# Kernel tuning notes

Hardware: AMD Instinct MI355X
Metric: run time of the kernel (lower is better)

## Reference

```python
import jax, jax.numpy as jnp
import numpy as np

TEMPERATURE = 0.5  # init kwarg; forward's temperature arg is unused in the original

def _l2norm(x, eps=1e-12):
    # matches F.normalize(dim=-1)
    n = jnp.sqrt(jnp.sum(x * x, axis=-1, keepdims=True))
    return x / jnp.maximum(n, eps)

def setup_inputs() -> dict:
    key = jax.random.key(0)
    k1, k2 = jax.random.split(key)
    h1 = jax.random.normal(k1, (8192, 128), dtype=jnp.float32)
    h2 = jax.random.normal(k2, (8192, 128), dtype=jnp.float32)
    return {"h1": h1, "h2": h2}

def reference(h1, h2):
    t = TEMPERATURE
    h1n = _l2norm(h1)
    h2n = _l2norm(h2)
    h = jnp.concatenate([h1n, h2n], axis=0)              # [2N, d]
    sim = jnp.exp(jnp.matmul(h, h.T) / t)                # [2N, 2N]
    # masked_select of off-diagonal then row-sum == full row-sum minus diagonal
    denom = jnp.sum(sim, axis=-1) - jnp.diagonal(sim)    # [2N]
    pos = jnp.exp(jnp.sum(h1n * h2n, axis=-1) / t)       # [N]
    pos = jnp.concatenate([pos, pos], axis=0)            # [2N]
    loss = -jnp.log(pos / denom)
    return jnp.mean(loss)
```

## Files before the change

kernel.cpp:

```cpp
#include <hip/hip_runtime.h>
#include <hip/hip_bf16.h>

#define N_ROWS 8192
#define DIM    128
#define TWO_N  16384
#define NBLK   64
#define NTRI   (NBLK * (NBLK + 1) / 2)
#define CT     32
#define NT_SQ  8
#define EXP_TWO 7.38905609893065f
#define H_SCALE 1.6986436f

typedef __attribute__((ext_vector_type(8))) short short8;
typedef __attribute__((ext_vector_type(4))) float float4v;

__device__ inline void async_copy16(const void* g, void* l) {
  __builtin_amdgcn_global_load_lds(
      (const __attribute__((address_space(1))) void*)g,
      (__attribute__((address_space(3))) void*)l, 16, 0, 0);
}

__device__ inline float fast_exp2(float x) {
#if __has_builtin(__builtin_amdgcn_exp2f)
  return __builtin_amdgcn_exp2f(x);
#else
  return exp2f(x);
#endif
}

__global__ __launch_bounds__(256) void norm_kernel(
    const float* __restrict__ h1, const float* __restrict__ h2,
    __hip_bfloat16* __restrict__ Hb, float* __restrict__ posdot,
    float* __restrict__ rowsum) {
  if (threadIdx.x < 8) rowsum[blockIdx.x * 8 + threadIdx.x] = 0.0f;

  int lane = threadIdx.x & 63;
  int w    = threadIdx.x >> 6;
  int row  = blockIdx.x * 4 + w;

  const float2* p1 = (const float2*)(h1 + (size_t)row * DIM);
  const float2* p2 = (const float2*)(h2 + (size_t)row * DIM);
  float2 v1 = p1[lane];
  float2 v2 = p2[lane];

  float ss1 = v1.x * v1.x + v1.y * v1.y;
  float ss2 = v2.x * v2.x + v2.y * v2.y;
  #pragma unroll
  for (int m = 32; m; m >>= 1) {
    ss1 += __shfl_xor(ss1, m);
    ss2 += __shfl_xor(ss2, m);
  }
  float inv1 = 1.0f / fmaxf(sqrtf(ss1), 1e-12f);
  float inv2 = 1.0f / fmaxf(sqrtf(ss2), 1e-12f);

  float ax = v1.x * inv1, ay = v1.y * inv1;
  float bx = v2.x * inv2, by = v2.y * inv2;

  float pd = ax * bx + ay * by;
  #pragma unroll
  for (int m = 32; m; m >>= 1) pd += __shfl_xor(pd, m);

  __hip_bfloat162* o1 = (__hip_bfloat162*)(Hb + (size_t)row * DIM);
  __hip_bfloat162* o2 = (__hip_bfloat162*)(Hb + (size_t)(row + N_ROWS) * DIM);
  __hip_bfloat162 t1, t2;
  t1.x = __float2bfloat16(ax * H_SCALE); t1.y = __float2bfloat16(ay * H_SCALE);
  t2.x = __float2bfloat16(bx * H_SCALE); t2.y = __float2bfloat16(by * H_SCALE);
  o1[lane] = t1;
  o2[lane] = t2;

  if (lane == 0) posdot[row] = pd;
}

__global__ __launch_bounds__(256, 2) void ntx_main(
    const __hip_bfloat16* __restrict__ Hb, float* __restrict__ rowsum) {
  __shared__ short smem[2 * 4096];
  __shared__ float colacc[4][256];
  const short* H = (const short*)Hb;

  int tid  = threadIdx.x;
  int lane = tid & 63;
  int w    = tid >> 6;
  int q    = lane >> 4;
  int m    = lane & 15;

  int t = blockIdx.x;
  int I = (int)((129.0f - sqrtf(129.0f * 129.0f - 8.0f * (float)t)) * 0.5f);
  while ((I + 1) * (129 - (I + 1)) / 2 <= t) ++I;
  while (I * (129 - I) / 2 > t) --I;
  int J = I + (t - I * (129 - I) / 2);
  bool diag = (I == J);

  int rowbase = I * 256 + w * 64;
  int colbase = J * 256;

  short8 a[4][4];
  #pragma unroll
  for (int r = 0; r < 4; ++r)
    #pragma unroll
    for (int s = 0; s < 4; ++s)
      a[r][s] = *(const short8*)(H + (size_t)(rowbase + r * 16 + m) * DIM + s * 32 + q * 8);
  #pragma unroll
  for (int r = 0; r < 4; ++r)
    #pragma unroll
    for (int s = 0; s < 4; ++s)
      asm volatile("" : "+v"(a[r][s]));

  float rowacc[4][4];
  #pragma unroll
  for (int r = 0; r < 4; ++r)
    #pragma unroll
    for (int i = 0; i < 4; ++i) rowacc[r][i] = 0.0f;

  int i0 = tid, i1 = tid + 256;
  int c0 = i0 >> 8, s0 = (i0 >> 6) & 3, f0 = i0 & 15, q0 = (i0 >> 4) & 3;
  int c1 = i1 >> 8, s1 = (i1 >> 6) & 3, f1 = i1 & 15, q1 = (i1 >> 4) & 3;
  const short* ga = H + (size_t)(colbase + c0 * 16 + f0) * DIM + s0 * 32 + q0 * 8;
  const short* gb = H + (size_t)(colbase + c1 * 16 + f1) * DIM + s1 * 32 + q1 * 8;

  async_copy16(ga, (void*)&smem[i0 * 8]);
  async_copy16(gb, (void*)&smem[i1 * 8]);
  __syncthreads();

  int buf = 0;
  for (int ct = 0; ct < NT_SQ; ++ct) {
    if (ct + 1 < NT_SQ) {
      ga += CT * DIM;
      gb += CT * DIM;
      int d = (buf ^ 1) * 4096;
      async_copy16(ga, (void*)&smem[d + i0 * 8]);
      async_copy16(gb, (void*)&smem[d + i1 * 8]);
    }

    const short* bsrc = &smem[buf * 4096];
    #pragma unroll
    for (int c = 0; c < 2; ++c) {
      short8 b[4];
      #pragma unroll
      for (int s = 0; s < 4; ++s)
        b[s] = *(const short8*)&bsrc[(c * 256 + s * 64 + lane) * 8];
      float cp = 0.0f;
      #pragma unroll
      for (int r = 0; r < 4; ++r) {
        float4v acc = {0.f, 0.f, 0.f, 0.f};
        #pragma unroll
        for (int s = 0; s < 4; ++s)
          acc = __builtin_amdgcn_mfma_f32_16x16x32_bf16(a[r][s], b[s], acc, 0, 0, 0);
        #pragma unroll
        for (int i = 0; i < 4; ++i) {
          float e = fast_exp2(acc[i]);
          rowacc[r][i] += e;
          cp += e;
        }
      }
      if (!diag) {
        cp += __shfl_xor(cp, 16);
        cp += __shfl_xor(cp, 32);
        if (q == 0) colacc[w][ct * 32 + c * 16 + m] = cp;
      }
    }
    __syncthreads();
    buf ^= 1;
  }

  #pragma unroll
  for (int r = 0; r < 4; ++r)
    #pragma unroll
    for (int i = 0; i < 4; ++i) {
      float v = rowacc[r][i];
      v += __shfl_xor(v, 1);
      v += __shfl_xor(v, 2);
      v += __shfl_xor(v, 4);
      v += __shfl_xor(v, 8);
      rowacc[r][i] = v;
    }
  if (m == 0) {
    #pragma unroll
    for (int r = 0; r < 4; ++r)
      #pragma unroll
      for (int i = 0; i < 4; ++i)
        atomicAdd(&rowsum[rowbase + r * 16 + q * 4 + i], rowacc[r][i]);
  }

  if (!diag) {
    float v = colacc[0][tid] + colacc[1][tid] + colacc[2][tid] + colacc[3][tid];
    atomicAdd(&rowsum[colbase + tid], v);
  }
}

__global__ __launch_bounds__(1024) void finalize(
    const float* __restrict__ rowsum, const float* __restrict__ posdot,
    float* __restrict__ out) {
  __shared__ float red[32];
  int tid = threadIdx.x;
  float ld = 0.0f, pp = 0.0f;
  for (int i = tid; i < TWO_N; i += 1024) ld += logf(rowsum[i] - EXP_TWO);
  for (int i = tid; i < N_ROWS; i += 1024) pp += posdot[i];
  #pragma unroll
  for (int m = 32; m; m >>= 1) {
    ld += __shfl_xor(ld, m);
    pp += __shfl_xor(pp, m);
  }
  if ((tid & 63) == 0) {
    red[tid >> 6] = ld;
    red[16 + (tid >> 6)] = pp;
  }
  __syncthreads();
  if (tid == 0) {
    float tl = 0.0f, tp = 0.0f;
    #pragma unroll
    for (int i = 0; i < 16; ++i) { tl += red[i]; tp += red[16 + i]; }
    *out = (tl - 4.0f * tp) / (float)TWO_N;
  }
}

extern "C" void kernel_launch(void* const* d_in, const int* in_sizes, int n_in,
                              void* d_out, int out_size, void* d_ws, size_t ws_size,
                              hipStream_t stream) {
  const float* h1 = (const float*)d_in[0];
  const float* h2 = (const float*)d_in[1];
  char* ws = (char*)d_ws;

  __hip_bfloat16* Hb = (__hip_bfloat16*)ws;
  float* rowsum      = (float*)(ws + 4194304);
  float* posdot      = (float*)(ws + 4194304 + 65536);
  float* out         = (float*)d_out;

  norm_kernel<<<N_ROWS / 4, 256, 0, stream>>>(h1, h2, Hb, posdot, rowsum);
  ntx_main<<<NTRI, 256, 0, stream>>>(Hb, rowsum);
  finalize<<<1, 1024, 0, stream>>>(rowsum, posdot, out);
}
```

Before: 132.6 us.

## Load column tiles directly into registers instead of LDS double buffering

The main kernel no longer stages B column tiles through LDS with async global-to-LDS copies and per-tile barriers. Each wave now loads its B fragments straight from global memory into registers, double-buffered in software, which drops the __syncthreads per tile. The occupancy hint is raised to 3 blocks per CU, and a barrier is added before the column-accumulator reduction. The finalize kernel is vectorized with float4 loads. In exchange, every wave now reads the same column data from global/L2 on its own instead of sharing it through LDS, and it may use more registers.

```diff
diff --git a/kernel.cpp b/kernel.cpp
--- a/kernel.cpp
+++ b/kernel.cpp
@@ -6,19 +6,11 @@
 #define TWO_N  16384
 #define NBLK   64
 #define NTRI   (NBLK * (NBLK + 1) / 2)
-#define CT     32
-#define NT_SQ  8
 #define EXP_TWO 7.38905609893065f
 #define H_SCALE 1.6986436f
 
 typedef __attribute__((ext_vector_type(8))) short short8;
 typedef __attribute__((ext_vector_type(4))) float float4v;
-
-__device__ inline void async_copy16(const void* g, void* l) {
-  __builtin_amdgcn_global_load_lds(
-      (const __attribute__((address_space(1))) void*)g,
-      (__attribute__((address_space(3))) void*)l, 16, 0, 0);
-}
 
 __device__ inline float fast_exp2(float x) {
 #if __has_builtin(__builtin_amdgcn_exp2f)
@@ -71,9 +63,8 @@
   if (lane == 0) posdot[row] = pd;
 }
 
-__global__ __launch_bounds__(256, 2) void ntx_main(
+__global__ __launch_bounds__(256, 3) void ntx_main(
     const __hip_bfloat16* __restrict__ Hb, float* __restrict__ rowsum) {
-  __shared__ short smem[2 * 4096];
   __shared__ float colacc[4][256];
   const short* H = (const short*)Hb;
 
@@ -111,56 +102,49 @@
     #pragma unroll
     for (int i = 0; i < 4; ++i) rowacc[r][i] = 0.0f;
 
-  int i0 = tid, i1 = tid + 256;
-  int c0 = i0 >> 8, s0 = (i0 >> 6) & 3, f0 = i0 & 15, q0 = (i0 >> 4) & 3;
-  int c1 = i1 >> 8, s1 = (i1 >> 6) & 3, f1 = i1 & 15, q1 = (i1 >> 4) & 3;
-  const short* ga = H + (size_t)(colbase + c0 * 16 + f0) * DIM + s0 * 32 + q0 * 8;
-  const short* gb = H + (size_t)(colbase + c1 * 16 + f1) * DIM + s1 * 32 + q1 * 8;
-
-  async_copy16(ga, (void*)&smem[i0 * 8]);
-  async_copy16(gb, (void*)&smem[i1 * 8]);
-  __syncthreads();
-
-  int buf = 0;
-  for (int ct = 0; ct < NT_SQ; ++ct) {
-    if (ct + 1 < NT_SQ) {
-      ga += CT * DIM;
-      gb += CT * DIM;
-      int d = (buf ^ 1) * 4096;
-      async_copy16(ga, (void*)&smem[d + i0 * 8]);
-      async_copy16(gb, (void*)&smem[d + i1 * 8]);
-    }
-
-    const short* bsrc = &smem[buf * 4096];
-    #pragma unroll
-    for (int c = 0; c < 2; ++c) {
-      short8 b[4];
-      #pragma unroll
-      for (int s = 0; s < 4; ++s)
-        b[s] = *(const short8*)&bsrc[(c * 256 + s * 64 + lane) * 8];
-      float cp = 0.0f;
-      #pragma unroll
-      for (int r = 0; r < 4; ++r) {
-        float4v acc = {0.f, 0.f, 0.f, 0.f};
-        #pragma unroll
-        for (int s = 0; s < 4; ++s)
-          acc = __builtin_amdgcn_mfma_f32_16x16x32_bf16(a[r][s], b[s], acc, 0, 0, 0);
-        #pragma unroll
-        for (int i = 0; i < 4; ++i) {
-          float e = fast_exp2(acc[i]);
-          rowacc[r][i] += e;
-          cp += e;
-        }
-      }
-      if (!diag) {
-        cp += __shfl_xor(cp, 16);
-        cp += __shfl_xor(cp, 32);
-        if (q == 0) colacc[w][ct * 32 + c * 16 + m] = cp;
-      }
-    }
-    __syncthreads();
-    buf ^= 1;
-  }
+  const short* gp = H + (size_t)(colbase + m) * DIM + q * 8;
+
+#define LOADB(bb, ptr) do {                         \
+    bb[0] = *(const short8*)((ptr));                \
+    bb[1] = *(const short8*)((ptr) + 32);           \
+    bb[2] = *(const short8*)((ptr) + 64);           \
+    bb[3] = *(const short8*)((ptr) + 96);           \
+  } while (0)
+
+#define COMPUTE(bb, cs_) do {                                              \
+    float cp = 0.0f;                                                       \
+    _Pragma("unroll")                                                      \
+    for (int r = 0; r < 4; ++r) {                                          \
+      float4v acc = {0.f, 0.f, 0.f, 0.f};                                  \
+      _Pragma("unroll")                                                    \
+      for (int s = 0; s < 4; ++s)                                          \
+        acc = __builtin_amdgcn_mfma_f32_16x16x32_bf16(a[r][s], bb[s], acc, 0, 0, 0); \
+      _Pragma("unroll")                                                    \
+      for (int i = 0; i < 4; ++i) {                                        \
+        float e = fast_exp2(acc[i]);        \
+        rowacc[r][i] += e;                                                 \
+        cp += e;                                                           \
+      }                                                                    \
+    }                                                                      \
+    if (!diag) {                                                           \
+      cp += __shfl_xor(cp, 16);                                           \
+      cp += __shfl_xor(cp, 32);                                           \
+      if (q == 0) colacc[w][(cs_) * 16 + m] = cp;                          \
+    }                                                                      \
+  } while (0)
+
+  short8 b0[4], b1[4];
+  LOADB(b0, gp);
+  #pragma unroll 1
+  for (int cs = 0; cs < 16; cs += 2) {
+    LOADB(b1, gp + 16 * DIM);
+    COMPUTE(b0, cs);
+    gp += 32 * DIM;
+    if (cs + 2 < 16) LOADB(b0, gp);
+    COMPUTE(b1, cs + 1);
+  }
+#undef LOADB
+#undef COMPUTE
 
   #pragma unroll
   for (int r = 0; r < 4; ++r)
@@ -182,6 +166,7 @@
   }
 
   if (!diag) {
+    __syncthreads();
     float v = colacc[0][tid] + colacc[1][tid] + colacc[2][tid] + colacc[3][tid];
     atomicAdd(&rowsum[colbase + tid], v);
   }
@@ -192,9 +177,20 @@
     float* __restrict__ out) {
   __shared__ float red[32];
   int tid = threadIdx.x;
+  const float4* rs4 = (const float4*)rowsum;
+  const float4* pd4 = (const float4*)posdot;
   float ld = 0.0f, pp = 0.0f;
-  for (int i = tid; i < TWO_N; i += 1024) ld += logf(rowsum[i] - EXP_TWO);
-  for (int i = tid; i < N_ROWS; i += 1024) pp += posdot[i];
+  #pragma unroll
+  for (int it = 0; it < 4; ++it) {
+    float4 v = rs4[tid + it * 1024];
+    ld += logf(v.x - EXP_TWO) + logf(v.y - EXP_TWO) +
+          logf(v.z - EXP_TWO) + logf(v.w - EXP_TWO);
+  }
+  #pragma unroll
+  for (int it = 0; it < 2; ++it) {
+    float4 v = pd4[tid + it * 1024];
+    pp += v.x + v.y + v.z + v.w;
+  }
   #pragma unroll
   for (int m = 32; m; m >>= 1) {
     ld += __shfl_xor(ld, m);
```

Result: slower. 151.8 us (+14.5%).
